# Kernel tuning notes

Measured on AMD Instinct MI355X. Metric: run time of the kernel, lower is better.

## Reference

```python
import jax, jax.numpy as jnp
import numpy as np

EMB = 768
HEADS = 8
HEAD_DIM = EMB // HEADS
SCALE = HEAD_DIM ** -0.5


def setup_inputs() -> dict:
    key = jax.random.key(0)
    ks = jax.random.split(key, 9)
    s = EMB ** -0.5
    return {
        "x": jax.random.normal(ks[0], (2, 4096, EMB), dtype=jnp.float32),
        "Wq": jax.random.normal(ks[1], (EMB, EMB), dtype=jnp.float32) * s,
        "bq": jax.random.normal(ks[2], (EMB,), dtype=jnp.float32) * 0.02,
        "Wk": jax.random.normal(ks[3], (EMB, EMB), dtype=jnp.float32) * s,
        "bk": jax.random.normal(ks[4], (EMB,), dtype=jnp.float32) * 0.02,
        "Wv": jax.random.normal(ks[5], (EMB, EMB), dtype=jnp.float32) * s,
        "bv": jax.random.normal(ks[6], (EMB,), dtype=jnp.float32) * 0.02,
        "Wo": jax.random.normal(ks[7], (EMB, EMB), dtype=jnp.float32) * s,
        "bo": jax.random.normal(ks[8], (EMB,), dtype=jnp.float32) * 0.02,
    }


def reference(x, Wq, bq, Wk, bk, Wv, bv, Wo, bo):
    b, n, _ = x.shape
    def split_heads(t):  # [b, n, emb] -> [b, h, n, d]
        return t.reshape(b, n, HEADS, HEAD_DIM).transpose(0, 2, 1, 3)
    q = split_heads(x @ Wq + bq)
    k = split_heads(x @ Wk + bk)
    v = split_heads(x @ Wv + bv)
    scores = jnp.einsum('bhqd,bhkd->bhqk', q, k)
    # NOTE: faithful to source — softmax first, THEN multiply by scale.
    attn = jax.nn.softmax(scores, axis=-1) * SCALE
    out = jnp.einsum('bhqk,bhkd->bhqd', attn, v)
    out = out.transpose(0, 2, 1, 3).reshape(b, n, EMB)
    return out @ Wo + bo
```

## Files before the change

kernel.cpp:

```cpp
#include <hip/hip_runtime.h>
#include <hip/hip_fp16.h>


typedef _Float16 half8 __attribute__((ext_vector_type(8)));
typedef _Float16 half4 __attribute__((ext_vector_type(4)));
typedef float   float4_ __attribute__((ext_vector_type(4)));
typedef float   f32x16 __attribute__((ext_vector_type(16)));

#define SCALE 0.102062072615966f
#define LOG2E 1.44269504088896340736f

__device__ __forceinline__ float4_ mfma16(half8 a, half8 b, float4_ c) {
    return __builtin_amdgcn_mfma_f32_16x16x32_f16(a, b, c, 0, 0, 0);
}
__device__ __forceinline__ f32x16 mfma32(half8 a, half8 b, f32x16 c) {
    return __builtin_amdgcn_mfma_f32_32x32x16_f16(a, b, c, 0, 0, 0);
}
__device__ __forceinline__ void gload16(const _Float16* g, _Float16* l) {
    __builtin_amdgcn_global_load_lds(
        (const __attribute__((address_space(1))) void*)g,
        (__attribute__((address_space(3))) void*)l, 16, 0, 0);
}

__device__ __forceinline__ float fast_exp2(float x) {
#if __has_builtin(__builtin_amdgcn_exp2f)
    return __builtin_amdgcn_exp2f(x);
#else
    float r;
    asm("v_exp_f32 %0, %1" : "=v"(r) : "v"(x));
    return r;
#endif
}


__global__ void cast_x(const float* __restrict__ x, _Float16* __restrict__ xb) {
    int i = blockIdx.x * 256 + threadIdx.x;
    float4_ v = ((const float4_*)x)[i];
    half4 h = { (_Float16)v[0], (_Float16)v[1], (_Float16)v[2], (_Float16)v[3] };
    ((half4*)xb)[i] = h;
}

__global__ void prep_w(const float* __restrict__ Wq, const float* __restrict__ Wk,
                       const float* __restrict__ Wv, const float* __restrict__ Wo,
                       _Float16* __restrict__ wqkv, _Float16* __restrict__ wot) {
    __shared__ float tile[64][65];
    const int bid = blockIdx.x;
    const int mat = bid / 144, rem = bid % 144;
    const int kt = rem / 12, ct = rem % 12;
    const float* W = (mat == 0) ? Wq : (mat == 1) ? Wk : (mat == 2) ? Wv : Wo;
    const int k0 = kt * 64, c0 = ct * 64;
    const int t = threadIdx.x;
    const int lr = t >> 4, lc = (t & 15) * 4;
    #pragma unroll
    for (int i = 0; i < 4; ++i) {
        float4_ v = *(const float4_*)(W + (size_t)(k0 + i * 16 + lr) * 768 + c0 + lc);
        tile[i * 16 + lr][lc + 0] = v[0];
        tile[i * 16 + lr][lc + 1] = v[1];
        tile[i * 16 + lr][lc + 2] = v[2];
        tile[i * 16 + lr][lc + 3] = v[3];
    }
    __syncthreads();
    const int cr = t >> 2, kq = (t & 3) * 16;
    _Float16* dst = (mat < 3) ? (wqkv + ((size_t)(mat * 768 + c0 + cr)) * 768 + k0 + kq)
                              : (wot  + ((size_t)(c0 + cr)) * 768 + k0 + kq);
    half8 h0, h1;
    #pragma unroll
    for (int j = 0; j < 8; ++j) {
        h0[j] = (_Float16)tile[kq + j][cr];
        h1[j] = (_Float16)tile[kq + 8 + j][cr];
    }
    *(half8*)dst = h0;
    *(half8*)(dst + 8) = h1;
}

__global__ void prep_bias(const float* __restrict__ bq, const float* __restrict__ bk,
                          const float* __restrict__ bv, float* __restrict__ bqkv) {
    int i = blockIdx.x * 256 + threadIdx.x;
    float v = (i < 768) ? bq[i] : (i < 1536) ? bk[i - 768] : bv[i - 1536];
    bqkv[i] = v;
}

__global__ __launch_bounds__(256, 2) void gemm_kernel(
    const _Float16* __restrict__ A, const _Float16* __restrict__ Bt,
    const float* __restrict__ bias, int mode,
    _Float16* __restrict__ Qo, _Float16* __restrict__ Ko, _Float16* __restrict__ Vto,
    float* __restrict__ out)
{
    __shared__ alignas(16) _Float16 Af[16 * 512];
    __shared__ alignas(16) _Float16 Bf[16 * 512];
    const int tid = threadIdx.x;
    const int lane = tid & 63, w = tid >> 6;
    const int wm = w >> 1, wn = w & 1;
    const int l15 = lane & 15, l4 = lane >> 4;
    const int m0 = blockIdx.y * 128;
    const int n0 = blockIdx.x * 128;

    const _Float16* gs[8];
    _Float16* ld[8];
    #pragma unroll
    for (int i = 0; i < 8; ++i) {
        int f = (w & 1) * 8 + i;
        int rg = f >> 1, kc = f & 1;
        int r0 = ((w < 2) ? m0 : n0) + rg * 16;
        gs[i] = ((w < 2) ? A : Bt) + (size_t)(r0 + l15) * 768 + kc * 32 + l4 * 8;
        ld[i] = ((w < 2) ? Af : Bf) + f * 512;
    }

    float4_ acc[4][4] = {};

    for (int k0 = 0; k0 < 768; k0 += 64) {
        #pragma unroll
        for (int i = 0; i < 8; ++i)
            gload16(gs[i] + k0, ld[i]);
        __syncthreads();
        #pragma unroll
        for (int kc = 0; kc < 2; ++kc) {
            half8 bfr[4];
            #pragma unroll
            for (int nt = 0; nt < 4; ++nt)
                bfr[nt] = *(const half8*)(Bf + (size_t)(((wn * 4 + nt) * 2 + kc) * 512 + lane * 8));
            #pragma unroll
            for (int mt = 0; mt < 4; ++mt) {
                half8 afr = *(const half8*)(Af + (size_t)(((wm * 4 + mt) * 2 + kc) * 512 + lane * 8));
                #pragma unroll
                for (int nt = 0; nt < 4; ++nt)
                    acc[mt][nt] = mfma16(afr, bfr[nt], acc[mt][nt]);
            }
        }
        __syncthreads();
    }

    #pragma unroll
    for (int mt = 0; mt < 4; ++mt)
    #pragma unroll
    for (int nt = 0; nt < 4; ++nt) {
        int gc = n0 + wn * 64 + nt * 16 + l15;
        float bv_ = bias[gc];
        #pragma unroll
        for (int r = 0; r < 4; ++r) {
            int gm = m0 + wm * 64 + mt * 16 + l4 * 4 + r;
            float val = acc[mt][nt][r] + bv_;
            if (mode == 1) {
                out[(size_t)gm * 768 + gc] = val;
            } else {
                int b = gm >> 12, n = gm & 4095;
                if (gc < 768) {
                    int h = gc / 96, d = gc % 96;
                    Qo[(((size_t)(b * 8 + h)) * 4096 + n) * 96 + d] = (_Float16)(val * LOG2E);
                } else if (gc < 1536) {
                    int c = gc - 768, h = c / 96, d = c % 96;
                    int bh = b * 8 + h;
                    size_t idx = (((size_t)bh * 128 + (n >> 5)) * 6 + (d >> 4)) * 512
                               + (size_t)((d >> 3) & 1) * 256 + (size_t)(n & 31) * 8 + (d & 7);
                    Ko[idx] = (_Float16)val;
                } else {
                    int c = gc - 1536, h = c / 96, d = c % 96;
                    int bh = b * 8 + h;
                    size_t idx = (((size_t)bh * 64 + (n >> 6)) * 12 + ((n >> 4) & 3) * 3 + (d >> 5)) * 512
                               + (size_t)((n >> 3) & 1) * 256 + (size_t)(d & 31) * 8 + (n & 7);
                    Vto[idx] = (_Float16)val;
                }
            }
        }
    }
}

__global__ __launch_bounds__(256, 2) void attn_kernel(
    const _Float16* __restrict__ Q, const _Float16* __restrict__ Kf,
    const _Float16* __restrict__ Vf, _Float16* __restrict__ AO)
{
    __shared__ alignas(16) _Float16 kvbuf[2][24 * 512];
    __shared__ float tab[4][32];

    const int tid = threadIdx.x;
    const int lane = tid & 63, w = tid >> 6;
    const int l31 = lane & 31, hi = lane >> 5;

    const int B = blockIdx.x;
    const int xcd = B & 7, j = B >> 3;
    const int bh = 2 * xcd + (j >> 5);
    const int qb = j & 31;
    const int q0 = qb * 128 + w * 32;

    const size_t qBase = (size_t)bh * 4096 * 96;
    const _Float16* kfb = Kf + (size_t)bh * 393216;
    const _Float16* vfb = Vf + (size_t)bh * 393216;

    half8 qf[6];
    #pragma unroll
    for (int dch = 0; dch < 6; ++dch)
        qf[dch] = *(const half8*)(Q + qBase + (size_t)(q0 + l31) * 96 + dch * 16 + hi * 8);

    f32x16 o0 = {}, o1 = {}, o2 = {};
    float m = -1e30f, l = 0.f;

    const int fbase = w * 6;
    const _Float16* gbase = ((fbase < 12) ? (kfb + (size_t)fbase * 512)
                                          : (vfb + (size_t)(fbase - 12) * 512)) + lane * 8;

    half8 streg[6], vreg[12];

    #pragma unroll
    for (int i = 0; i < 6; ++i)
        streg[i] = *(const half8*)(gbase + i * 512);
    #pragma unroll
    for (int i = 0; i < 6; ++i)
        *(half8*)(&kvbuf[0][(fbase + i) * 512 + lane * 8]) = streg[i];
    __syncthreads();

    int cur = 0;
    for (int t = 0; t < 64; ++t) {
        const int tn = (t + 1) & 63;
        #pragma unroll
        for (int i = 0; i < 6; ++i)
            streg[i] = *(const half8*)(gbase + (size_t)tn * 6144 + i * 512);

        const _Float16* kb = &kvbuf[cur][0];
        const _Float16* vb = &kvbuf[cur][12 * 512];

        f32x16 s0 = {}, s1 = {};
        __builtin_amdgcn_s_setprio(1);
        #pragma unroll
        for (int dch = 0; dch < 6; ++dch) {
            half8 k0 = *(const half8*)(kb + dch * 512 + lane * 8);
            half8 k1 = *(const half8*)(kb + (6 + dch) * 512 + lane * 8);
            s0 = mfma32(k0, qf[dch], s0);
            s1 = mfma32(k1, qf[dch], s1);
        }
        __builtin_amdgcn_s_setprio(0);

        #pragma unroll
        for (int i = 0; i < 12; ++i)
            vreg[i] = *(const half8*)(vb + i * 512 + lane * 8);

        float mx[8];
        #pragma unroll
        for (int r = 0; r < 8; ++r)
            mx[r] = fmaxf(fmaxf(s0[r], s0[r + 8]), fmaxf(s1[r], s1[r + 8]));
        mx[0] = fmaxf(mx[0], mx[4]); mx[1] = fmaxf(mx[1], mx[5]);
        mx[2] = fmaxf(mx[2], mx[6]); mx[3] = fmaxf(mx[3], mx[7]);
        float lm = fmaxf(fmaxf(mx[0], mx[1]), fmaxf(mx[2], mx[3]));
        float pmax = fmaxf(lm, __shfl_xor(lm, 32));
        if (__any(pmax > m + 8.0f)) {
            float mn = fmaxf(m, pmax);
            float al = fast_exp2(m - mn);
            m = mn; l *= al;
            if (hi == 0) tab[w][l31] = al;
            asm volatile("s_waitcnt lgkmcnt(0)" ::: "memory");
            #pragma unroll
            for (int r = 0; r < 16; ++r) {
                float alr = tab[w][(r & 3) + 8 * (r >> 2) + 4 * hi];
                o0[r] *= alr; o1[r] *= alr; o2[r] *= alr;
            }
        }
        float ls = 0.f;
        uint32_t Lp[16];
        #pragma unroll
        for (int kg = 0; kg < 2; ++kg) {
            const f32x16& s = kg ? s1 : s0;
            #pragma unroll
            for (int jg = 0; jg < 4; ++jg) {
                float p0 = fast_exp2(s[4 * jg + 0] - m);
                float p1 = fast_exp2(s[4 * jg + 1] - m);
                float p2 = fast_exp2(s[4 * jg + 2] - m);
                float p3 = fast_exp2(s[4 * jg + 3] - m);
                ls += (p0 + p1) + (p2 + p3);
                union { _Float16 h[2]; uint32_t u; } pk0, pk1;
                pk0.h[0] = (_Float16)p0; pk0.h[1] = (_Float16)p1;
                pk1.h[0] = (_Float16)p2; pk1.h[1] = (_Float16)p3;
                Lp[kg * 8 + jg * 2] = pk0.u; Lp[kg * 8 + jg * 2 + 1] = pk1.u;
            }
        }
        l += ls + __shfl_xor(ls, 32);

        half8 pa[4];
        #pragma unroll
        for (int kk = 0; kk < 4; ++kk) {
            uint32_t u0 = Lp[4 * kk], u1 = Lp[4 * kk + 1];
            uint32_t u2 = Lp[4 * kk + 2], u3 = Lp[4 * kk + 3];
            asm("v_permlane32_swap_b32 %0, %1" : "+v"(u0), "+v"(u2));
            asm("v_permlane32_swap_b32 %0, %1" : "+v"(u1), "+v"(u3));
            union { half8 h; uint32_t u[4]; } fr;
            fr.u[0] = u0; fr.u[1] = u1; fr.u[2] = u2; fr.u[3] = u3;
            pa[kk] = fr.h;
        }

        __builtin_amdgcn_s_setprio(1);
        #pragma unroll
        for (int kk = 0; kk < 4; ++kk) {
            o0 = mfma32(pa[kk], vreg[kk * 3 + 0], o0);
            o1 = mfma32(pa[kk], vreg[kk * 3 + 1], o1);
            o2 = mfma32(pa[kk], vreg[kk * 3 + 2], o2);
        }
        __builtin_amdgcn_s_setprio(0);

        __syncthreads();
        #pragma unroll
        for (int i = 0; i < 6; ++i)
            *(half8*)(&kvbuf[cur ^ 1][(fbase + i) * 512 + lane * 8]) = streg[i];
        __syncthreads();
        cur ^= 1;
    }

    if (hi == 0) tab[w][l31] = l;
    asm volatile("s_waitcnt lgkmcnt(0)" ::: "memory");
    const int b = bh >> 3, h = bh & 7;
    #pragma unroll
    for (int r = 0; r < 16; ++r) {
        int qrow = (r & 3) + 8 * (r >> 2) + 4 * hi;
        float inv = SCALE / tab[w][qrow];
        int n = q0 + qrow;
        size_t base = ((size_t)(b * 4096 + n)) * 768 + h * 96 + l31;
        AO[base]      = (_Float16)(o0[r] * inv);
        AO[base + 32] = (_Float16)(o1[r] * inv);
        AO[base + 64] = (_Float16)(o2[r] * inv);
    }
}


extern "C" void kernel_launch(void* const* d_in, const int* in_sizes, int n_in,
                              void* d_out, int out_size, void* d_ws, size_t ws_size,
                              hipStream_t stream) {
    const float* x  = (const float*)d_in[0];
    const float* Wq = (const float*)d_in[1];
    const float* bq = (const float*)d_in[2];
    const float* Wk = (const float*)d_in[3];
    const float* bk = (const float*)d_in[4];
    const float* Wv = (const float*)d_in[5];
    const float* bv = (const float*)d_in[6];
    const float* Wo = (const float*)d_in[7];
    const float* bo = (const float*)d_in[8];
    float* out = (float*)d_out;

    char* ws = (char*)d_ws;
    _Float16* xb   = (_Float16*)(ws);
    _Float16* wqkv = (_Float16*)(ws + 12582912);
    _Float16* wot  = (_Float16*)(ws + 16121856);
    float*    bqkv = (float*)   (ws + 17301504);
    _Float16* Qb   = (_Float16*)(ws + 17310720);
    _Float16* Kfb  = (_Float16*)(ws + 29893632);
    _Float16* Vfb  = (_Float16*)(ws + 42476544);
    _Float16* AO   = xb;

    cast_x<<<6144, 256, 0, stream>>>(x, xb);
    prep_w<<<576, 256, 0, stream>>>(Wq, Wk, Wv, Wo, wqkv, wot);
    prep_bias<<<9, 256, 0, stream>>>(bq, bk, bv, bqkv);

    gemm_kernel<<<dim3(18, 64), 256, 0, stream>>>(xb, wqkv, bqkv, 0, Qb, Kfb, Vfb, nullptr);

    attn_kernel<<<512, 256, 0, stream>>>(Qb, Kfb, Vfb, AO);

    gemm_kernel<<<dim3(6, 64), 256, 0, stream>>>(AO, wot, bo, 1, nullptr, nullptr, nullptr, out);
}
```

Before: 254.7 us.

## Split KV sequence across two wave groups per block and merge partial softmax

The attention kernel now runs 512 threads per block. Two groups of four waves each process half of the key/value sequence for the same 128 queries, with 32-key tiles instead of 64. At the end, the partial max, sum and output of the two halves are merged through shared memory. This raises the number of waves per CU to hide latency. In exchange it adds an end-of-kernel reduction and more barrier traffic, and it drops the double-buffered KV staging in favour of a single buffer per half.

```diff
diff --git a/kernel.cpp b/kernel.cpp
--- a/kernel.cpp
+++ b/kernel.cpp
@@ -165,26 +165,29 @@
     }
 }
 
-__global__ __launch_bounds__(256, 2) void attn_kernel(
+__global__ __launch_bounds__(512, 4) void attn_kernel(
     const _Float16* __restrict__ Q, const _Float16* __restrict__ Kf,
     const _Float16* __restrict__ Vf, _Float16* __restrict__ AO)
 {
-    __shared__ alignas(16) _Float16 kvbuf[2][24 * 512];
-    __shared__ float tab[4][32];
+    __shared__ alignas(16) float shm4[12288];
+    __shared__ float tab[8][32];
+    __shared__ float mtab[4][2][32], ltab[4][2][32], wtab[4][2][32], lftab[4][32];
+
+    _Float16* stage = (_Float16*)shm4;
 
     const int tid = threadIdx.x;
     const int lane = tid & 63, w = tid >> 6;
     const int l31 = lane & 31, hi = lane >> 5;
+    const int p = w & 3, half = w >> 2;
 
     const int B = blockIdx.x;
     const int xcd = B & 7, j = B >> 3;
     const int bh = 2 * xcd + (j >> 5);
     const int qb = j & 31;
-    const int q0 = qb * 128 + w * 32;
+    const int q0 = qb * 128 + p * 32;
 
     const size_t qBase = (size_t)bh * 4096 * 96;
-    const _Float16* kfb = Kf + (size_t)bh * 393216;
-    const _Float16* vfb = Vf + (size_t)bh * 393216;
+    const size_t kvHalf = (size_t)bh * 393216 + (size_t)half * 196608;
 
     half8 qf[6];
     #pragma unroll
@@ -194,51 +197,48 @@
     f32x16 o0 = {}, o1 = {}, o2 = {};
     float m = -1e30f, l = 0.f;
 
-    const int fbase = w * 6;
-    const _Float16* gbase = ((fbase < 12) ? (kfb + (size_t)fbase * 512)
-                                          : (vfb + (size_t)(fbase - 12) * 512)) + lane * 8;
-
-    half8 streg[6], vreg[12];
-
-    #pragma unroll
-    for (int i = 0; i < 6; ++i)
-        streg[i] = *(const half8*)(gbase + i * 512);
-    #pragma unroll
-    for (int i = 0; i < 6; ++i)
-        *(half8*)(&kvbuf[0][(fbase + i) * 512 + lane * 8]) = streg[i];
-    __syncthreads();
-
-    int cur = 0;
+    const int f0 = p * 3;
+    const _Float16* gsrc[3];
+    #pragma unroll
+    for (int i = 0; i < 3; ++i) {
+        int f = f0 + i;
+        gsrc[i] = ((f < 6) ? Kf : Vf) + kvHalf + (size_t)((f < 6) ? f : f - 6) * 512 + lane * 8;
+    }
+    _Float16* sbase = stage + half * 6144;
+
+    half8 streg[3], vreg[6];
+
+    #pragma unroll
+    for (int i = 0; i < 3; ++i)
+        streg[i] = *(const half8*)(gsrc[i]);
+    #pragma unroll
+    for (int i = 0; i < 3; ++i)
+        *(half8*)(sbase + (f0 + i) * 512 + lane * 8) = streg[i];
+    __syncthreads();
+
     for (int t = 0; t < 64; ++t) {
         const int tn = (t + 1) & 63;
         #pragma unroll
+        for (int i = 0; i < 3; ++i)
+            streg[i] = *(const half8*)(gsrc[i] + (size_t)tn * 3072);
+
+        f32x16 s = {};
+        __builtin_amdgcn_s_setprio(1);
+        #pragma unroll
+        for (int dch = 0; dch < 6; ++dch) {
+            half8 k0 = *(const half8*)(sbase + dch * 512 + lane * 8);
+            s = mfma32(k0, qf[dch], s);
+        }
+        __builtin_amdgcn_s_setprio(0);
+
+        #pragma unroll
         for (int i = 0; i < 6; ++i)
-            streg[i] = *(const half8*)(gbase + (size_t)tn * 6144 + i * 512);
-
-        const _Float16* kb = &kvbuf[cur][0];
-        const _Float16* vb = &kvbuf[cur][12 * 512];
-
-        f32x16 s0 = {}, s1 = {};
-        __builtin_amdgcn_s_setprio(1);
-        #pragma unroll
-        for (int dch = 0; dch < 6; ++dch) {
-            half8 k0 = *(const half8*)(kb + dch * 512 + lane * 8);
-            half8 k1 = *(const half8*)(kb + (6 + dch) * 512 + lane * 8);
-            s0 = mfma32(k0, qf[dch], s0);
-            s1 = mfma32(k1, qf[dch], s1);
-        }
-        __builtin_amdgcn_s_setprio(0);
-
-        #pragma unroll
-        for (int i = 0; i < 12; ++i)
-            vreg[i] = *(const half8*)(vb + i * 512 + lane * 8);
-
-        float mx[8];
-        #pragma unroll
-        for (int r = 0; r < 8; ++r)
-            mx[r] = fmaxf(fmaxf(s0[r], s0[r + 8]), fmaxf(s1[r], s1[r + 8]));
-        mx[0] = fmaxf(mx[0], mx[4]); mx[1] = fmaxf(mx[1], mx[5]);
-        mx[2] = fmaxf(mx[2], mx[6]); mx[3] = fmaxf(mx[3], mx[7]);
+            vreg[i] = *(const half8*)(sbase + (6 + i) * 512 + lane * 8);
+
+        float mx[4];
+        #pragma unroll
+        for (int r = 0; r < 4; ++r)
+            mx[r] = fmaxf(fmaxf(s[r], s[r + 4]), fmaxf(s[r + 8], s[r + 12]));
         float lm = fmaxf(fmaxf(mx[0], mx[1]), fmaxf(mx[2], mx[3]));
         float pmax = fmaxf(lm, __shfl_xor(lm, 32));
         if (__any(pmax > m + 8.0f)) {
@@ -254,28 +254,24 @@
             }
         }
         float ls = 0.f;
-        uint32_t Lp[16];
-        #pragma unroll
-        for (int kg = 0; kg < 2; ++kg) {
-            const f32x16& s = kg ? s1 : s0;
-            #pragma unroll
-            for (int jg = 0; jg < 4; ++jg) {
-                float p0 = fast_exp2(s[4 * jg + 0] - m);
-                float p1 = fast_exp2(s[4 * jg + 1] - m);
-                float p2 = fast_exp2(s[4 * jg + 2] - m);
-                float p3 = fast_exp2(s[4 * jg + 3] - m);
-                ls += (p0 + p1) + (p2 + p3);
-                union { _Float16 h[2]; uint32_t u; } pk0, pk1;
-                pk0.h[0] = (_Float16)p0; pk0.h[1] = (_Float16)p1;
-                pk1.h[0] = (_Float16)p2; pk1.h[1] = (_Float16)p3;
-                Lp[kg * 8 + jg * 2] = pk0.u; Lp[kg * 8 + jg * 2 + 1] = pk1.u;
-            }
+        uint32_t Lp[8];
+        #pragma unroll
+        for (int jg = 0; jg < 4; ++jg) {
+            float p0 = fast_exp2(s[4 * jg + 0] - m);
+            float p1 = fast_exp2(s[4 * jg + 1] - m);
+            float p2 = fast_exp2(s[4 * jg + 2] - m);
+            float p3 = fast_exp2(s[4 * jg + 3] - m);
+            ls += (p0 + p1) + (p2 + p3);
+            union { _Float16 h[2]; uint32_t u; } pk0, pk1;
+            pk0.h[0] = (_Float16)p0; pk0.h[1] = (_Float16)p1;
+            pk1.h[0] = (_Float16)p2; pk1.h[1] = (_Float16)p3;
+            Lp[jg * 2] = pk0.u; Lp[jg * 2 + 1] = pk1.u;
         }
         l += ls + __shfl_xor(ls, 32);
 
-        half8 pa[4];
-        #pragma unroll
-        for (int kk = 0; kk < 4; ++kk) {
+        half8 pa[2];
+        #pragma unroll
+        for (int kk = 0; kk < 2; ++kk) {
             uint32_t u0 = Lp[4 * kk], u1 = Lp[4 * kk + 1];
             uint32_t u2 = Lp[4 * kk + 2], u3 = Lp[4 * kk + 3];
             asm("v_permlane32_swap_b32 %0, %1" : "+v"(u0), "+v"(u2));
@@ -287,7 +283,7 @@
 
         __builtin_amdgcn_s_setprio(1);
         #pragma unroll
-        for (int kk = 0; kk < 4; ++kk) {
+        for (int kk = 0; kk < 2; ++kk) {
             o0 = mfma32(pa[kk], vreg[kk * 3 + 0], o0);
             o1 = mfma32(pa[kk], vreg[kk * 3 + 1], o1);
             o2 = mfma32(pa[kk], vreg[kk * 3 + 2], o2);
@@ -296,24 +292,50 @@
 
         __syncthreads();
         #pragma unroll
-        for (int i = 0; i < 6; ++i)
-            *(half8*)(&kvbuf[cur ^ 1][(fbase + i) * 512 + lane * 8]) = streg[i];
+        for (int i = 0; i < 3; ++i)
+            *(half8*)(sbase + (f0 + i) * 512 + lane * 8) = streg[i];
         __syncthreads();
-        cur ^= 1;
-    }
-
-    if (hi == 0) tab[w][l31] = l;
-    asm volatile("s_waitcnt lgkmcnt(0)" ::: "memory");
-    const int b = bh >> 3, h = bh & 7;
-    #pragma unroll
-    for (int r = 0; r < 16; ++r) {
-        int qrow = (r & 3) + 8 * (r >> 2) + 4 * hi;
-        float inv = SCALE / tab[w][qrow];
-        int n = q0 + qrow;
-        size_t base = ((size_t)(b * 4096 + n)) * 768 + h * 96 + l31;
-        AO[base]      = (_Float16)(o0[r] * inv);
-        AO[base + 32] = (_Float16)(o1[r] * inv);
-        AO[base + 64] = (_Float16)(o2[r] * inv);
+    }
+
+    if (hi == 0) { mtab[p][half][l31] = m; ltab[p][half][l31] = l; }
+    __syncthreads();
+    {
+        float mA = mtab[p][0][l31], mB = mtab[p][1][l31];
+        float lA = ltab[p][0][l31], lB = ltab[p][1][l31];
+        float M = fmaxf(mA, mB);
+        float wA_ = fast_exp2(mA - M), wB_ = fast_exp2(mB - M);
+        if (hi == 0) {
+            wtab[p][half][l31] = half ? wB_ : wA_;
+            if (half == 0) lftab[p][l31] = lA * wA_ + lB * wB_;
+        }
+    }
+    __syncthreads();
+    if (half == 1) {
+        #pragma unroll
+        for (int r = 0; r < 16; ++r) {
+            int qr = (r & 3) + 8 * (r >> 2) + 4 * hi;
+            float wr = wtab[p][1][qr];
+            float* ob = &shm4[p * 3072 + qr * 96 + l31];
+            ob[0]  = o0[r] * wr;
+            ob[32] = o1[r] * wr;
+            ob[64] = o2[r] * wr;
+        }
+    }
+    __syncthreads();
+    if (half == 0) {
+        const int b = bh >> 3, h = bh & 7;
+        #pragma unroll
+        for (int r = 0; r < 16; ++r) {
+            int qr = (r & 3) + 8 * (r >> 2) + 4 * hi;
+            float wr = wtab[p][0][qr];
+            float inv = SCALE / lftab[p][qr];
+            const float* ob = &shm4[p * 3072 + qr * 96 + l31];
+            int n = q0 + qr;
+            size_t base = ((size_t)(b * 4096 + n)) * 768 + h * 96 + l31;
+            AO[base]      = (_Float16)((o0[r] * wr + ob[0])  * inv);
+            AO[base + 32] = (_Float16)((o1[r] * wr + ob[32]) * inv);
+            AO[base + 64] = (_Float16)((o2[r] * wr + ob[64]) * inv);
+        }
     }
 }
 
@@ -348,7 +370,7 @@
 
     gemm_kernel<<<dim3(18, 64), 256, 0, stream>>>(xb, wqkv, bqkv, 0, Qb, Kfb, Vfb, nullptr);
 
-    attn_kernel<<<512, 256, 0, stream>>>(Qb, Kfb, Vfb, AO);
+    attn_kernel<<<512, 512, 0, stream>>>(Qb, Kfb, Vfb, AO);
 
     gemm_kernel<<<dim3(6, 64), 256, 0, stream>>>(AO, wot, bo, 1, nullptr, nullptr, nullptr, out);
 }
```

Measured after the change: 395.2 us. +55.1%, slower.

## Process two KV tiles per iteration with a single LDS buffer

Applied to the files above, without the earlier changes.

The attention loop now stages two 64-key KV tiles per iteration into one 48-chunk LDS buffer, in place of double-buffering single tiles. Both QK^T products are issued back to back before the two softmax/PV phases, and V fragments are loaded from LDS right before each PV MFMA. This halves the number of loop iterations and barrier pairs and gives the scheduler more independent MFMA work. In exchange it doubles the staging registers and drops the double buffering, so the LDS store of the next tile now waits behind a full barrier.

```diff
diff --git a/kernel.cpp b/kernel.cpp
--- a/kernel.cpp
+++ b/kernel.cpp
@@ -169,7 +169,7 @@
     const _Float16* __restrict__ Q, const _Float16* __restrict__ Kf,
     const _Float16* __restrict__ Vf, _Float16* __restrict__ AO)
 {
-    __shared__ alignas(16) _Float16 kvbuf[2][24 * 512];
+    __shared__ alignas(16) _Float16 kvbuf[48 * 512];
     __shared__ float tab[4][32];
 
     const int tid = threadIdx.x;
@@ -198,41 +198,9 @@
     const _Float16* gbase = ((fbase < 12) ? (kfb + (size_t)fbase * 512)
                                           : (vfb + (size_t)(fbase - 12) * 512)) + lane * 8;
 
-    half8 streg[6], vreg[12];
-
-    #pragma unroll
-    for (int i = 0; i < 6; ++i)
-        streg[i] = *(const half8*)(gbase + i * 512);
-    #pragma unroll
-    for (int i = 0; i < 6; ++i)
-        *(half8*)(&kvbuf[0][(fbase + i) * 512 + lane * 8]) = streg[i];
-    __syncthreads();
-
-    int cur = 0;
-    for (int t = 0; t < 64; ++t) {
-        const int tn = (t + 1) & 63;
-        #pragma unroll
-        for (int i = 0; i < 6; ++i)
-            streg[i] = *(const half8*)(gbase + (size_t)tn * 6144 + i * 512);
-
-        const _Float16* kb = &kvbuf[cur][0];
-        const _Float16* vb = &kvbuf[cur][12 * 512];
-
-        f32x16 s0 = {}, s1 = {};
-        __builtin_amdgcn_s_setprio(1);
-        #pragma unroll
-        for (int dch = 0; dch < 6; ++dch) {
-            half8 k0 = *(const half8*)(kb + dch * 512 + lane * 8);
-            half8 k1 = *(const half8*)(kb + (6 + dch) * 512 + lane * 8);
-            s0 = mfma32(k0, qf[dch], s0);
-            s1 = mfma32(k1, qf[dch], s1);
-        }
-        __builtin_amdgcn_s_setprio(0);
-
-        #pragma unroll
-        for (int i = 0; i < 12; ++i)
-            vreg[i] = *(const half8*)(vb + i * 512 + lane * 8);
-
+    half8 streg[12];
+
+    auto softmax_pa = [&](const f32x16& s0, const f32x16& s1, half8* pa) {
         float mx[8];
         #pragma unroll
         for (int r = 0; r < 8; ++r)
@@ -272,8 +240,6 @@
             }
         }
         l += ls + __shfl_xor(ls, 32);
-
-        half8 pa[4];
         #pragma unroll
         for (int kk = 0; kk < 4; ++kk) {
             uint32_t u0 = Lp[4 * kk], u1 = Lp[4 * kk + 1];
@@ -284,22 +250,86 @@
             fr.u[0] = u0; fr.u[1] = u1; fr.u[2] = u2; fr.u[3] = u3;
             pa[kk] = fr.h;
         }
-
+    };
+
+    #pragma unroll
+    for (int i = 0; i < 6; ++i) {
+        streg[i]     = *(const half8*)(gbase + i * 512);
+        streg[6 + i] = *(const half8*)(gbase + 6144 + i * 512);
+    }
+    #pragma unroll
+    for (int i = 0; i < 6; ++i) {
+        *(half8*)(&kvbuf[(fbase + i) * 512 + lane * 8])      = streg[i];
+        *(half8*)(&kvbuf[(24 + fbase + i) * 512 + lane * 8]) = streg[6 + i];
+    }
+    __syncthreads();
+
+    for (int t = 0; t < 32; ++t) {
+        const int tn = (t + 1) & 31;
+        const size_t goff = (size_t)tn * 12288;
+        #pragma unroll
+        for (int i = 0; i < 6; ++i) {
+            streg[i]     = *(const half8*)(gbase + goff + i * 512);
+            streg[6 + i] = *(const half8*)(gbase + goff + 6144 + i * 512);
+        }
+
+        const _Float16* kbA = &kvbuf[0];
+        const _Float16* vbA = &kvbuf[12 * 512];
+        const _Float16* kbB = &kvbuf[24 * 512];
+        const _Float16* vbB = &kvbuf[36 * 512];
+
+        f32x16 sA0 = {}, sA1 = {}, sB0 = {}, sB1 = {};
         __builtin_amdgcn_s_setprio(1);
         #pragma unroll
+        for (int dch = 0; dch < 6; ++dch) {
+            half8 k0 = *(const half8*)(kbA + dch * 512 + lane * 8);
+            half8 k1 = *(const half8*)(kbA + (6 + dch) * 512 + lane * 8);
+            sA0 = mfma32(k0, qf[dch], sA0);
+            sA1 = mfma32(k1, qf[dch], sA1);
+        }
+        #pragma unroll
+        for (int dch = 0; dch < 6; ++dch) {
+            half8 k0 = *(const half8*)(kbB + dch * 512 + lane * 8);
+            half8 k1 = *(const half8*)(kbB + (6 + dch) * 512 + lane * 8);
+            sB0 = mfma32(k0, qf[dch], sB0);
+            sB1 = mfma32(k1, qf[dch], sB1);
+        }
+        __builtin_amdgcn_s_setprio(0);
+
+        half8 pa[4];
+        softmax_pa(sA0, sA1, pa);
+        __builtin_amdgcn_s_setprio(1);
+        #pragma unroll
         for (int kk = 0; kk < 4; ++kk) {
-            o0 = mfma32(pa[kk], vreg[kk * 3 + 0], o0);
-            o1 = mfma32(pa[kk], vreg[kk * 3 + 1], o1);
-            o2 = mfma32(pa[kk], vreg[kk * 3 + 2], o2);
+            half8 v0 = *(const half8*)(vbA + (kk * 3 + 0) * 512 + lane * 8);
+            half8 v1 = *(const half8*)(vbA + (kk * 3 + 1) * 512 + lane * 8);
+            half8 v2 = *(const half8*)(vbA + (kk * 3 + 2) * 512 + lane * 8);
+            o0 = mfma32(pa[kk], v0, o0);
+            o1 = mfma32(pa[kk], v1, o1);
+            o2 = mfma32(pa[kk], v2, o2);
         }
         __builtin_amdgcn_s_setprio(0);
 
+        softmax_pa(sB0, sB1, pa);
+        __builtin_amdgcn_s_setprio(1);
+        #pragma unroll
+        for (int kk = 0; kk < 4; ++kk) {
+            half8 v0 = *(const half8*)(vbB + (kk * 3 + 0) * 512 + lane * 8);
+            half8 v1 = *(const half8*)(vbB + (kk * 3 + 1) * 512 + lane * 8);
+            half8 v2 = *(const half8*)(vbB + (kk * 3 + 2) * 512 + lane * 8);
+            o0 = mfma32(pa[kk], v0, o0);
+            o1 = mfma32(pa[kk], v1, o1);
+            o2 = mfma32(pa[kk], v2, o2);
+        }
+        __builtin_amdgcn_s_setprio(0);
+
         __syncthreads();
         #pragma unroll
-        for (int i = 0; i < 6; ++i)
-            *(half8*)(&kvbuf[cur ^ 1][(fbase + i) * 512 + lane * 8]) = streg[i];
+        for (int i = 0; i < 6; ++i) {
+            *(half8*)(&kvbuf[(fbase + i) * 512 + lane * 8])      = streg[i];
+            *(half8*)(&kvbuf[(24 + fbase + i) * 512 + lane * 8]) = streg[6 + i];
+        }
         __syncthreads();
-        cur ^= 1;
     }
 
     if (hi == 0) tab[w][l31] = l;
```

Result: no change. 255.7 us (+0.4%).
